# Kernel tuning notes

Measured on AMD Instinct MI355X. Metric: run time of the kernel, lower is better.

## Reference

```python
import jax, jax.numpy as jnp
import numpy as np

ORDER = 2
HIDDEN = 64
INPUT_SIZE = 2
N_NODES = 1024
BATCH = 8
STEPS = 32
GN_EPS = 1e-5


def setup_inputs() -> dict:
    key = jax.random.key(0)
    ks = jax.random.split(key, 8)
    c_gate_in = INPUT_SIZE + HIDDEN            # channels of concat([x, h]) fed to gate convs
    n_supp = 2 * ORDER                          # fwd/bwd row-normalized adj + (order-1) powers each
    c_conv = (n_supp + 1) * c_gate_in           # include_self=True adds the identity (self) block

    def w(k, shape, fan_in):
        s = 1.0 / np.sqrt(fan_in)
        return jax.random.uniform(k, shape, jnp.float32, -s, s)

    return {
        "x":   jax.random.normal(ks[0], (BATCH, INPUT_SIZE, N_NODES, STEPS), jnp.float32),
        "adj": jax.random.uniform(ks[1], (N_NODES, N_NODES), jnp.float32),
        "h0":  jax.random.normal(ks[2], (HIDDEN, N_NODES), jnp.float32) / np.sqrt(HIDDEN),
        "Wr": w(ks[3], (HIDDEN, c_conv), c_conv), "br": jnp.zeros((HIDDEN,), jnp.float32),
        "Wu": w(ks[4], (HIDDEN, c_conv), c_conv), "bu": jnp.zeros((HIDDEN,), jnp.float32),
        "Wc": w(ks[5], (HIDDEN, c_conv), c_conv), "bc": jnp.zeros((HIDDEN,), jnp.float32),
        "gamma": jnp.ones((HIDDEN,), jnp.float32), "beta": jnp.zeros((HIDDEN,), jnp.float32),
        "Wo": w(ks[6], (INPUT_SIZE, HIDDEN), HIDDEN), "bo": jnp.zeros((INPUT_SIZE,), jnp.float32),
    }


def _supports(adj, order):
    # SpatialConvOrderK.compute_support_orderK(adj, K, include_self=True)
    fwd = adj / (adj.sum(1, keepdims=True) + 1e-8)
    bwd = adj.T / (adj.T.sum(1, keepdims=True) + 1e-8)
    supp = [fwd, bwd]
    for a in (fwd, bwd):
        ak = a
        for _ in range(order - 1):
            ak = ak @ a.T               # higher-order diffusion; include_self -> keep diagonal
            supp.append(ak)
    return jnp.stack(supp)              # [S, n, n], S = 2*order


def _gconv(z, supp, W, b):
    # order-1 graph conv over precomputed order-K supports, include_self=True
    # z: [b, c, n]; supp: [S, n, n]; torch: einsum('ncvl,wv->ncwl')
    agg = jnp.einsum('bcv,swv->bscw', z, supp)            # [b, S, c, n]
    zc = jnp.concatenate([z[:, None], agg], axis=1)       # [b, S+1, c, n] (self first)
    zc = zc.reshape(z.shape[0], -1, z.shape[2])           # [b, (S+1)*c, n]
    return jnp.einsum('oc,bcn->bon', W, zc) + b[None, :, None]


def _gnorm(h, gamma, beta):
    # GroupNorm(num_groups=1): normalize each sample over (channels, nodes)
    m = h.mean(axis=(1, 2), keepdims=True)
    v = ((h - m) ** 2).mean(axis=(1, 2), keepdims=True)
    return (h - m) * jax.lax.rsqrt(v + GN_EPS) * gamma[None, :, None] + beta[None, :, None]


def reference(x, adj, h0, Wr, br, Wu, bu, Wc, bc, gamma, beta, Wo, bo):
    supp = _supports(adj, ORDER)
    b, _, n, _ = x.shape
    h = jnp.broadcast_to(h0[None], (b, HIDDEN, n))
    xs = jnp.moveaxis(x, -1, 0)                           # [steps, b, c_in, n]

    def step(h, xt):
        zg = jnp.concatenate([xt, h], axis=1)             # [b, c_in+hidden, n]
        r = jax.nn.sigmoid(_gconv(zg, supp, Wr, br))      # reset gate
        u = jax.nn.sigmoid(_gconv(zg, supp, Wu, bu))      # update gate
        zc = jnp.concatenate([xt, r * h], axis=1)
        c = jnp.tanh(_gconv(zc, supp, Wc, bc))            # candidate
        hn = _gnorm(u * h + (1.0 - u) * c, gamma, beta)   # norm applied post-cell (h[layer] = norm(...))
        x_hat = jnp.einsum('oc,bcn->bon', Wo, hn) + bo[None, :, None]  # first_stage 1x1 conv
        return hn, (x_hat, hn)

    _, (imps, hs) = jax.lax.scan(step, h, xs)
    imputations = jnp.moveaxis(imps, 0, -1)               # [b, input_size, n, steps]
    states = jnp.moveaxis(hs, 0, -1)[None]                # [n_layers=1, b, hidden, n, steps]
    return imputations, states
```

## Files before the change

kernel.cpp:

```cpp
#include <hip/hip_runtime.h>
#include <math.h>

#define NN 1024
#define HID 64
#define CIN 2
#define BB 8
#define TT 32
#define CG 66
#define NBC 528
#define K2 384
#define GN_EPS 1e-5f
#define LDAP 72

typedef __attribute__((ext_vector_type(8))) short short8v;
typedef __attribute__((ext_vector_type(4))) float float4v;

#define GLD16(gp, lp) __builtin_amdgcn_global_load_lds( \
    (const __attribute__((address_space(1))) void*)(gp), \
    (__attribute__((address_space(3))) void*)(lp), 16, 0, 0)

__device__ __forceinline__ unsigned short f2b(float v) {
    union { float f; unsigned int u; } a; a.f = v;
    unsigned int r = a.u + 0x7FFFu + ((a.u >> 16) & 1u);
    return (unsigned short)(r >> 16);
}
__device__ __forceinline__ float b2f(unsigned short b) {
    union { unsigned int u; float f; } a; a.u = ((unsigned int)b) << 16;
    return a.f;
}
__device__ __forceinline__ float sigmoidf_(float v) { return 1.f / (1.f + __expf(-v)); }

__device__ __forceinline__ float wave_reduce_sum(float v) {
    #pragma unroll
    for (int o = 32; o > 0; o >>= 1) v += __shfl_down(v, o, 64);
    return v;
}


__global__ void rowsum_k(const float* __restrict__ adj, float* __restrict__ rs) {
    int i = blockIdx.x;
    float s = 0.f;
    for (int j = threadIdx.x; j < NN; j += 256) s += adj[(size_t)i * NN + j];
    s = wave_reduce_sum(s);
    __shared__ float sh[4];
    int wid = threadIdx.x >> 6, lid = threadIdx.x & 63;
    if (lid == 0) sh[wid] = s;
    __syncthreads();
    if (threadIdx.x == 0) rs[i] = sh[0] + sh[1] + sh[2] + sh[3];
}

__global__ void colsum_k(const float* __restrict__ adj, float* __restrict__ cpart) {
    int j = (blockIdx.x & 3) * 256 + threadIdx.x;
    int r0 = (blockIdx.x >> 2) * 128;
    float s = 0.f;
    for (int i = 0; i < 128; i++) s += adj[(size_t)(r0 + i) * NN + j];
    cpart[(size_t)(blockIdx.x >> 2) * NN + j] = s;
}

__global__ void fwdb_k(const float* __restrict__ adj, const float* __restrict__ rs,
                       unsigned short* __restrict__ sb) {
    int idx = blockIdx.x * 256 + threadIdx.x;
    int i = idx >> 10;
    sb[idx] = f2b(adj[idx] / (rs[i] + 1e-8f));
}

__global__ void bwdb_k(const float* __restrict__ adj, const float* __restrict__ cpart,
                       unsigned short* __restrict__ sb) {
    __shared__ float tile[32][33];
    int i0 = blockIdx.y * 32, j0 = blockIdx.x * 32;
    int tx = threadIdx.x, ty = threadIdx.y;
    #pragma unroll
    for (int r = ty; r < 32; r += 8)
        tile[r][tx] = adj[(size_t)(j0 + r) * NN + i0 + tx];
    __syncthreads();
    #pragma unroll
    for (int r = ty; r < 32; r += 8) {
        int i = i0 + r;
        float cs = 0.f;
        #pragma unroll
        for (int c = 0; c < 8; c++) cs += cpart[(size_t)c * NN + i];
        sb[(size_t)i * NN + j0 + tx] = f2b(tile[tx][r] / (cs + 1e-8f));
    }
}

__global__ __launch_bounds__(256) void suppk_mfma(const unsigned short* __restrict__ sb,
                                                  unsigned short* __restrict__ outb) {
    int z = blockIdx.z;
    const unsigned short* A = sb + (size_t)z * NN * NN;
    unsigned short* D = outb + (size_t)z * NN * NN;
    __shared__ unsigned short lA[128 * LDAP];
    __shared__ unsigned short lB[64 * LDAP];
    int tid = threadIdx.x;
    int m0 = blockIdx.x * 128, n0 = blockIdx.y * 64;
    int lane = tid & 63, wave = tid >> 6;
    int wm = wave >> 1, wn = wave & 1;
    float4v acc[4][2];
    #pragma unroll
    for (int i = 0; i < 4; i++)
        #pragma unroll
        for (int j = 0; j < 2; j++) acc[i][j] = (float4v){0.f, 0.f, 0.f, 0.f};
    int lrow = lane & 15, lk8 = (lane >> 4) * 8;
    for (int k0 = 0; k0 < NN; k0 += 64) {
        #pragma unroll
        for (int s = 0; s < 4; s++) {
            int slot = tid + s * 256;
            int r = slot >> 3, kg = slot & 7;
            *(short8v*)(lA + r * LDAP + kg * 8) =
                *(const short8v*)(A + (size_t)(m0 + r) * NN + k0 + kg * 8);
        }
        #pragma unroll
        for (int s = 0; s < 2; s++) {
            int slot = tid + s * 256;
            int r = slot >> 3, kg = slot & 7;
            *(short8v*)(lB + r * LDAP + kg * 8) =
                *(const short8v*)(A + (size_t)(n0 + r) * NN + k0 + kg * 8);
        }
        __syncthreads();
        #pragma unroll
        for (int kk = 0; kk < 2; kk++) {
            short8v af[4], bf[2];
            #pragma unroll
            for (int i = 0; i < 4; i++)
                af[i] = *(const short8v*)(lA + (wm * 64 + i * 16 + lrow) * LDAP + kk * 32 + lk8);
            #pragma unroll
            for (int j = 0; j < 2; j++)
                bf[j] = *(const short8v*)(lB + (wn * 32 + j * 16 + lrow) * LDAP + kk * 32 + lk8);
            #pragma unroll
            for (int i = 0; i < 4; i++)
                #pragma unroll
                for (int j = 0; j < 2; j++)
                    acc[i][j] = __builtin_amdgcn_mfma_f32_16x16x32_bf16(af[i], bf[j], acc[i][j], 0, 0, 0);
        }
        __syncthreads();
    }
    int col = lane & 15, q4 = (lane >> 4) * 4;
    #pragma unroll
    for (int i = 0; i < 4; i++)
        #pragma unroll
        for (int j = 0; j < 2; j++) {
            int n = n0 + wn * 32 + j * 16 + col;
            #pragma unroll
            for (int r = 0; r < 4; r++) {
                int mm = m0 + wm * 64 + i * 16 + q4 + r;
                D[(size_t)mm * NN + n] = f2b(acc[i][j][r]);
            }
        }
}

__global__ void wconv_k(const float* __restrict__ Wr, const float* __restrict__ Wu,
                        const float* __restrict__ Wc, unsigned short* __restrict__ Wb,
                        unsigned short* __restrict__ Wcb) {
    int idx = blockIdx.x * 256 + threadIdx.x;
    int row = idx / K2, j = idx - row * K2;
    float v = 0.f;
    if (j < 330) {
        int q = j / CG, rr = j - q * CG;
        int chan = q * CG + (rr < HID ? rr + CIN : rr - HID);
        if (row < 64) v = Wr[row * 330 + chan];
        else if (row < 128) v = Wu[(row - 64) * 330 + chan];
        else v = Wc[(row - 128) * 330 + chan];
    }
    if (row < 128) Wb[row * K2 + j] = f2b(v);
    else Wcb[(row - 128) * K2 + j] = f2b(v);
}

__global__ void zeroz_k(unsigned short* __restrict__ z) {
    size_t i = ((size_t)blockIdx.x * 256 + threadIdx.x) * 8;
    *(short8v*)(z + i) = (short8v){0, 0, 0, 0, 0, 0, 0, 0};
}

__global__ void init_k(const float* __restrict__ x, const float* __restrict__ h0,
                       float* __restrict__ h, unsigned short* __restrict__ Z2g,
                       unsigned short* __restrict__ Z2c, unsigned short* __restrict__ Abfg,
                       unsigned short* __restrict__ Abfc) {
    int m = blockIdx.x * 256 + threadIdx.x;
    int b = m >> 10, n = m & 1023;
    for (int c = 0; c < HID; c++) {
        float v = h0[(c << 10) + n];
        h[(size_t)m * HID + c] = v;
        unsigned short hv = f2b(v);
        Z2g[(size_t)m * K2 + c] = hv;
        Abfg[(((size_t)(b * CG + c)) << 10) | n] = hv;
    }
    for (int o = 0; o < CIN; o++) {
        float xv = x[((((size_t)(b * CIN + o)) << 10) + n) * TT];
        unsigned short xb = f2b(xv);
        Z2g[(size_t)m * K2 + HID + o] = xb;
        Z2c[(size_t)m * K2 + HID + o] = xb;
        Abfg[(((size_t)(b * CG + HID + o)) << 10) | n] = xb;
        Abfc[(((size_t)(b * CG + HID + o)) << 10) | n] = xb;
    }
}


__global__ __launch_bounds__(256) void agg2_k(const unsigned short* __restrict__ S,
                                              const unsigned short* __restrict__ Abf,
                                              unsigned short* __restrict__ Z2) {
    __shared__ __align__(16) unsigned short lA[3][64 * 64];
    __shared__ __align__(16) unsigned short lB[3][64 * 64];
    int tid = threadIdx.x;
    int lin = blockIdx.y * 9 + blockIdx.x;
    int swz = (lin & 7) * 72 + (lin >> 3);
    int c0 = (swz % 9) * 64;
    int m0 = (swz / 9) * 64;
    int lane = tid & 63, wave = tid >> 6;
    int wm = wave >> 1, wn = wave & 1;
    float4v acc[2][2];
    #pragma unroll
    for (int i = 0; i < 2; i++)
        #pragma unroll
        for (int j = 0; j < 2; j++) acc[i][j] = (float4v){0.f, 0.f, 0.f, 0.f};
    int lrow = lane & 15, hi = lane >> 4;

    auto stage = [&](unsigned short* bufA, unsigned short* bufB, int k0) {
        #pragma unroll
        for (int i = 0; i < 2; i++) {
            int cid = (i * 4 + wave) * 64 + lane;
            int r = cid >> 3, sz = cid & 7;
            GLD16(S + (size_t)(m0 + r) * NN + k0 + ((sz ^ (r & 7)) << 3),
                  bufA + (i * 4 + wave) * 512);
        }
        #pragma unroll
        for (int i = 0; i < 2; i++) {
            int cid = (i * 4 + wave) * 64 + lane;
            int r = cid >> 3, sz = cid & 7;
            GLD16(Abf + (((size_t)(c0 + r)) << 10) + k0 + ((sz ^ (r & 7)) << 3),
                  bufB + (i * 4 + wave) * 512);
        }
    };

    unsigned short *a0 = lA[0], *a1 = lA[1], *a2 = lA[2];
    unsigned short *b0 = lB[0], *b1 = lB[1], *b2 = lB[2];
    stage(a0, b0, 0);
    stage(a1, b1, 64);
    for (int kt = 0; kt < 16; kt++) {
        if (kt < 15) asm volatile("s_waitcnt vmcnt(4)" ::: "memory");
        else         asm volatile("s_waitcnt vmcnt(0)" ::: "memory");
        __builtin_amdgcn_s_barrier();
        asm volatile("" ::: "memory");
        if (kt < 14) stage(a2, b2, (kt + 2) * 64);
        #pragma unroll
        for (int kk = 0; kk < 2; kk++) {
            int cb = kk * 4 + hi;
            short8v af[2], bf[2];
            #pragma unroll
            for (int i = 0; i < 2; i++) {
                int lr = wm * 32 + i * 16 + lrow;
                af[i] = *(const short8v*)(a0 + lr * 64 + ((cb ^ (lr & 7)) << 3));
            }
            #pragma unroll
            for (int j = 0; j < 2; j++) {
                int lr = wn * 32 + j * 16 + lrow;
                bf[j] = *(const short8v*)(b0 + lr * 64 + ((cb ^ (lr & 7)) << 3));
            }
            #pragma unroll
            for (int i = 0; i < 2; i++)
                #pragma unroll
                for (int j = 0; j < 2; j++)
                    acc[i][j] = __builtin_amdgcn_mfma_f32_16x16x32_bf16(af[i], bf[j], acc[i][j], 0, 0, 0);
        }
        { unsigned short* t = a0; a0 = a1; a1 = a2; a2 = t; }
        { unsigned short* t = b0; b0 = b1; b1 = b2; b2 = t; }
    }
    int col = lane & 15, q4 = (lane >> 4) * 4;
    int s_idx = m0 >> 10;
    int nb0 = (m0 & 1023) + wm * 32;
    #pragma unroll
    for (int j = 0; j < 2; j++) {
        int bc = c0 + wn * 32 + j * 16 + col;
        if (bc < NBC) {
            int b = bc / CG;
            int rr = bc - b * CG;
            size_t zcol = (size_t)CG + s_idx * CG + rr;
            #pragma unroll
            for (int i = 0; i < 2; i++) {
                int nb = nb0 + i * 16 + q4;
                #pragma unroll
                for (int r = 0; r < 4; r++)
                    Z2[((size_t)((b << 10) | (nb + r))) * K2 + zcol] = f2b(acc[i][j][r]);
            }
        }
    }
}

__global__ __launch_bounds__(256) void gates_k2(const unsigned short* __restrict__ Z2g,
                                                const unsigned short* __restrict__ Wb,
                                                const float* __restrict__ br,
                                                const float* __restrict__ bu,
                                                const float* __restrict__ h,
                                                float* __restrict__ u,
                                                unsigned short* __restrict__ Z2c,
                                                unsigned short* __restrict__ Abfc) {
    __shared__ __align__(16) unsigned short lA[3][32 * 64];
    __shared__ __align__(16) unsigned short lB[3][64 * 64];
    int tid = threadIdx.x;
    int m0 = blockIdx.x * 32;
    int isU = blockIdx.y;
    const unsigned short* W = Wb + (size_t)isU * 64 * K2;
    int lane = tid & 63, wave = tid >> 6;
    int wm = wave >> 1, wn = wave & 1;
    float4v acc[2];
    acc[0] = (float4v){0.f, 0.f, 0.f, 0.f};
    acc[1] = (float4v){0.f, 0.f, 0.f, 0.f};
    int lrow = lane & 15, hi = lane >> 4;

    auto stage = [&](unsigned short* bufA, unsigned short* bufB, int k0) {
        {
            int cid = wave * 64 + lane;
            int r = cid >> 3, sz = cid & 7;
            GLD16(Z2g + (size_t)(m0 + r) * K2 + k0 + ((sz ^ (r & 7)) << 3),
                  bufA + wave * 512);
        }
        #pragma unroll
        for (int i = 0; i < 2; i++) {
            int cid = (i * 4 + wave) * 64 + lane;
            int r = cid >> 3, sz = cid & 7;
            GLD16(W + (size_t)r * K2 + k0 + ((sz ^ (r & 7)) << 3),
                  bufB + (i * 4 + wave) * 512);
        }
    };

    unsigned short *a0 = lA[0], *a1 = lA[1], *a2 = lA[2];
    unsigned short *b0 = lB[0], *b1 = lB[1], *b2 = lB[2];
    stage(a0, b0, 0);
    stage(a1, b1, 64);
    for (int kt = 0; kt < 6; kt++) {
        if (kt < 5) asm volatile("s_waitcnt vmcnt(3)" ::: "memory");
        else        asm volatile("s_waitcnt vmcnt(0)" ::: "memory");
        __builtin_amdgcn_s_barrier();
        asm volatile("" ::: "memory");
        if (kt < 4) stage(a2, b2, (kt + 2) * 64);
        #pragma unroll
        for (int kk = 0; kk < 2; kk++) {
            int cb = kk * 4 + hi;
            short8v af, bf[2];
            {
                int lr = wm * 16 + lrow;
                af = *(const short8v*)(a0 + lr * 64 + ((cb ^ (lr & 7)) << 3));
            }
            #pragma unroll
            for (int j = 0; j < 2; j++) {
                int lr = wn * 32 + j * 16 + lrow;
                bf[j] = *(const short8v*)(b0 + lr * 64 + ((cb ^ (lr & 7)) << 3));
            }
            #pragma unroll
            for (int j = 0; j < 2; j++)
                acc[j] = __builtin_amdgcn_mfma_f32_16x16x32_bf16(af, bf[j], acc[j], 0, 0, 0);
        }
        { unsigned short* t = a0; a0 = a1; a1 = a2; a2 = t; }
        { unsigned short* t = b0; b0 = b1; b1 = b2; b2 = t; }
    }
    int col = lane & 15, q4 = (lane >> 4) * 4;
    #pragma unroll
    for (int j = 0; j < 2; j++) {
        int oo = wn * 32 + j * 16 + col;
        float bias = isU ? bu[oo] : br[oo];
        #pragma unroll
        for (int r = 0; r < 4; r++) {
            int m = m0 + wm * 16 + q4 + r;
            float g = sigmoidf_(acc[j][r] + bias);
            if (isU) {
                u[(size_t)m * HID + oo] = g;
            } else {
                float rh = g * h[(size_t)m * HID + oo];
                unsigned short hv = f2b(rh);
                Z2c[(size_t)m * K2 + oo] = hv;
                int b = m >> 10, n = m & 1023;
                Abfc[(((size_t)(b * CG + oo)) << 10) | n] = hv;
            }
        }
    }
}

__global__ __launch_bounds__(256) void cand_k2(const unsigned short* __restrict__ Z2c,
                                               const unsigned short* __restrict__ Wcb,
                                               const float* __restrict__ bcv,
                                               const float* __restrict__ u,
                                               const float* __restrict__ h,
                                               float* __restrict__ hraw,
                                               float* __restrict__ stats2, int t) {
    __shared__ __align__(16) unsigned short lA[3][32 * 64];
    __shared__ __align__(16) unsigned short lB[3][64 * 64];
    int tid = threadIdx.x;
    int m0 = blockIdx.x * 32;
    int lane = tid & 63, wave = tid >> 6;
    int wm = wave >> 1, wn = wave & 1;
    float4v acc[2];
    acc[0] = (float4v){0.f, 0.f, 0.f, 0.f};
    acc[1] = (float4v){0.f, 0.f, 0.f, 0.f};
    int lrow = lane & 15, hi = lane >> 4;

    auto stage = [&](unsigned short* bufA, unsigned short* bufB, int k0) {
        {
            int cid = wave * 64 + lane;
            int r = cid >> 3, sz = cid & 7;
            GLD16(Z2c + (size_t)(m0 + r) * K2 + k0 + ((sz ^ (r & 7)) << 3),
                  bufA + wave * 512);
        }
        #pragma unroll
        for (int i = 0; i < 2; i++) {
            int cid = (i * 4 + wave) * 64 + lane;
            int r = cid >> 3, sz = cid & 7;
            GLD16(Wcb + (size_t)r * K2 + k0 + ((sz ^ (r & 7)) << 3),
                  bufB + (i * 4 + wave) * 512);
        }
    };

    unsigned short *a0 = lA[0], *a1 = lA[1], *a2 = lA[2];
    unsigned short *b0 = lB[0], *b1 = lB[1], *b2 = lB[2];
    stage(a0, b0, 0);
    stage(a1, b1, 64);
    for (int kt = 0; kt < 6; kt++) {
        if (kt < 5) asm volatile("s_waitcnt vmcnt(3)" ::: "memory");
        else        asm volatile("s_waitcnt vmcnt(0)" ::: "memory");
        __builtin_amdgcn_s_barrier();
        asm volatile("" ::: "memory");
        if (kt < 4) stage(a2, b2, (kt + 2) * 64);
        #pragma unroll
        for (int kk = 0; kk < 2; kk++) {
            int cb = kk * 4 + hi;
            short8v af, bf[2];
            {
                int lr = wm * 16 + lrow;
                af = *(const short8v*)(a0 + lr * 64 + ((cb ^ (lr & 7)) << 3));
            }
            #pragma unroll
            for (int j = 0; j < 2; j++) {
                int lr = wn * 32 + j * 16 + lrow;
                bf[j] = *(const short8v*)(b0 + lr * 64 + ((cb ^ (lr & 7)) << 3));
            }
            #pragma unroll
            for (int j = 0; j < 2; j++)
                acc[j] = __builtin_amdgcn_mfma_f32_16x16x32_bf16(af, bf[j], acc[j], 0, 0, 0);
        }
        { unsigned short* t_ = a0; a0 = a1; a1 = a2; a2 = t_; }
        { unsigned short* t_ = b0; b0 = b1; b1 = b2; b2 = t_; }
    }
    int col = lane & 15, q4 = (lane >> 4) * 4;
    float ls = 0.f, ls2 = 0.f;
    #pragma unroll
    for (int j = 0; j < 2; j++) {
        int oo = wn * 32 + j * 16 + col;
        float bias = bcv[oo];
        #pragma unroll
        for (int r = 0; r < 4; r++) {
            int m = m0 + wm * 16 + q4 + r;
            float cv = tanhf(acc[j][r] + bias);
            float uv = u[(size_t)m * HID + oo];
            float hv = h[(size_t)m * HID + oo];
            float hr = uv * hv + (1.f - uv) * cv;
            hraw[(size_t)m * HID + oo] = hr;
            ls += hr;
            ls2 = fmaf(hr, hr, ls2);
        }
    }
    ls = wave_reduce_sum(ls);
    ls2 = wave_reduce_sum(ls2);
    __shared__ float sred[8];
    if (lane == 0) { sred[wave] = ls; sred[4 + wave] = ls2; }
    __syncthreads();
    if (tid == 0) {
        float S = sred[0] + sred[1] + sred[2] + sred[3];
        float S2 = sred[4] + sred[5] + sred[6] + sred[7];
        int b = blockIdx.x >> 5, slot = blockIdx.x & 31;
        float* dst = stats2 + (((size_t)t * BB + b) * 32 + slot) * 2;
        dst[0] = S;
        dst[1] = S2;
    }
}

__global__ __launch_bounds__(256) void apply_k2(const float* __restrict__ hraw,
                                                const float* __restrict__ stats2,
                                                const float* __restrict__ gamma,
                                                const float* __restrict__ beta,
                                                const float* __restrict__ Wo,
                                                const float* __restrict__ bo,
                                                const float* __restrict__ x,
                                                float* __restrict__ h,
                                                unsigned short* __restrict__ Z2g,
                                                unsigned short* __restrict__ Z2c,
                                                unsigned short* __restrict__ Abfg,
                                                unsigned short* __restrict__ Abfc,
                                                unsigned short* __restrict__ hseq8,
                                                float* __restrict__ iseq, int t) {
    int gid = blockIdx.x * 256 + threadIdx.x;
    int m = gid >> 3, q = gid & 7;
    int b = m >> 10, n = m & 1023;
    const float* st = stats2 + ((size_t)t * BB + b) * 64;
    float S = 0.f, S2 = 0.f;
    #pragma unroll
    for (int i = 0; i < 16; i++) {
        float4 p4 = *(const float4*)&st[i * 4];
        S += p4.x + p4.z;
        S2 += p4.y + p4.w;
    }
    float mean = S * (1.f / 65536.f);
    float rstd = rsqrtf(S2 * (1.f / 65536.f) - mean * mean + GN_EPS);
    bool more = (t < TT - 1);
    int c0 = q * 8;
    float v[8];
    unsigned short hb[8];
    #pragma unroll
    for (int k = 0; k < 8; k += 4) {
        float4 r4 = *(const float4*)&hraw[(size_t)m * HID + c0 + k];
        v[k + 0] = (r4.x - mean) * rstd * gamma[c0 + k + 0] + beta[c0 + k + 0];
        v[k + 1] = (r4.y - mean) * rstd * gamma[c0 + k + 1] + beta[c0 + k + 1];
        v[k + 2] = (r4.z - mean) * rstd * gamma[c0 + k + 2] + beta[c0 + k + 2];
        v[k + 3] = (r4.w - mean) * rstd * gamma[c0 + k + 3] + beta[c0 + k + 3];
    }
    float acc0 = 0.f, acc1 = 0.f;
    #pragma unroll
    for (int k = 0; k < 8; k++) {
        acc0 = fmaf(Wo[c0 + k], v[k], acc0);
        acc1 = fmaf(Wo[HID + c0 + k], v[k], acc1);
        hb[k] = f2b(v[k]);
    }
    short8v h8;
    #pragma unroll
    for (int k = 0; k < 8; k++) h8[k] = (short)hb[k];
    size_t hsbase = ((size_t)(t & 7) * 8192 + m) * HID + c0;
    *(short8v*)&hseq8[hsbase] = h8;
    if (more) {
        #pragma unroll
        for (int k = 0; k < 8; k += 4)
            *(float4*)&h[(size_t)m * HID + c0 + k] = make_float4(v[k], v[k + 1], v[k + 2], v[k + 3]);
        *(short8v*)&Z2g[(size_t)m * K2 + c0] = h8;
        #pragma unroll
        for (int k = 0; k < 8; k++)
            Abfg[(((size_t)(b * CG + c0 + k)) << 10) | n] = hb[k];
    }
    acc0 += __shfl_xor(acc0, 1, 64); acc0 += __shfl_xor(acc0, 2, 64); acc0 += __shfl_xor(acc0, 4, 64);
    acc1 += __shfl_xor(acc1, 1, 64); acc1 += __shfl_xor(acc1, 2, 64); acc1 += __shfl_xor(acc1, 4, 64);
    if (q == 0) {
        iseq[((size_t)t * 8192 + m) * 2 + 0] = acc0 + bo[0];
        iseq[((size_t)t * 8192 + m) * 2 + 1] = acc1 + bo[1];
        if (more) {
            #pragma unroll
            for (int o = 0; o < CIN; o++) {
                float xv = x[((((size_t)(b * CIN + o)) << 10) + n) * TT + t + 1];
                unsigned short xb = f2b(xv);
                Z2g[(size_t)m * K2 + HID + o] = xb;
                Z2c[(size_t)m * K2 + HID + o] = xb;
                Abfg[(((size_t)(b * CG + HID + o)) << 10) | n] = xb;
                Abfc[(((size_t)(b * CG + HID + o)) << 10) | n] = xb;
            }
        }
    }
}

__global__ __launch_bounds__(256) void strans_k(const unsigned short* __restrict__ hseq8,
                                                float* __restrict__ outS, int t0) {
    __shared__ unsigned short lt[8 * 576];
    int tid = threadIdx.x;
    int b = blockIdx.x >> 7;
    int n0 = (blockIdx.x & 127) * 8;
    #pragma unroll
    for (int s = 0; s < 2; s++) {
        int slot = tid + s * 256;
        int tt = slot >> 6, dn = (slot >> 3) & 7, kc = slot & 7;
        short8v vv = *(const short8v*)(hseq8 + ((size_t)tt * 8192 + ((b << 10) | (n0 + dn))) * HID + kc * 8);
        *(short8v*)(lt + tt * 576 + dn * 72 + kc * 8) = vv;
    }
    __syncthreads();
    #pragma unroll
    for (int s = 0; s < 2; s++) {
        int rid = tid + s * 256;
        int c = rid >> 3, dn = rid & 7;
        float f[8];
        #pragma unroll
        for (int tt = 0; tt < 8; tt++) f[tt] = b2f(lt[tt * 576 + dn * 72 + c]);
        float* dst = outS + ((((size_t)(b * HID + c)) << 10) + n0 + dn) * TT + t0;
        *(float4*)&dst[0] = make_float4(f[0], f[1], f[2], f[3]);
        *(float4*)&dst[4] = make_float4(f[4], f[5], f[6], f[7]);
    }
}

__global__ void itrans_k(const float* __restrict__ iseq, float* __restrict__ out) {
    int gid = blockIdx.x * 256 + threadIdx.x;
    int b = gid >> 11, o = (gid >> 10) & 1, n = gid & 1023;
    float f[TT];
    #pragma unroll
    for (int t = 0; t < TT; t++)
        f[t] = iseq[((size_t)t * 8192 + ((b << 10) | n)) * 2 + o];
    float* dst = out + ((((size_t)(b * CIN + o)) << 10) + n) * TT;
    #pragma unroll
    for (int k = 0; k < TT; k += 4)
        *(float4*)&dst[k] = make_float4(f[k], f[k + 1], f[k + 2], f[k + 3]);
}


extern "C" void kernel_launch(void* const* d_in, const int* in_sizes, int n_in,
                              void* d_out, int out_size, void* d_ws, size_t ws_size,
                              hipStream_t stream) {
    const float* x     = (const float*)d_in[0];
    const float* adj   = (const float*)d_in[1];
    const float* h0    = (const float*)d_in[2];
    const float* Wr    = (const float*)d_in[3];
    const float* br    = (const float*)d_in[4];
    const float* Wu    = (const float*)d_in[5];
    const float* bu    = (const float*)d_in[6];
    const float* Wc    = (const float*)d_in[7];
    const float* bcv   = (const float*)d_in[8];
    const float* gamma = (const float*)d_in[9];
    const float* beta  = (const float*)d_in[10];
    const float* Wo    = (const float*)d_in[11];
    const float* bo    = (const float*)d_in[12];
    float* out = (float*)d_out;

    char* p = (char*)d_ws;
    unsigned short* suppb = (unsigned short*)p;  p += (size_t)4 * NN * NN * 2;
    unsigned short* Abfg  = (unsigned short*)p;  p += (size_t)576 * NN * 2;
    unsigned short* Abfc  = (unsigned short*)p;  p += (size_t)576 * NN * 2;
    unsigned short* Z2g   = (unsigned short*)p;  p += (size_t)8192 * K2 * 2;
    unsigned short* Z2c   = (unsigned short*)p;  p += (size_t)8192 * K2 * 2;
    unsigned short* Wb    = (unsigned short*)p;  p += (size_t)128 * K2 * 2;
    unsigned short* Wcb   = (unsigned short*)p;  p += (size_t)64 * K2 * 2;
    float* u     = (float*)p;  p += (size_t)8192 * HID * 4;
    float* h     = (float*)p;  p += (size_t)8192 * HID * 4;
    float* hraw  = (float*)p;  p += (size_t)8192 * HID * 4;
    unsigned short* hseq8 = (unsigned short*)p;  p += (size_t)8 * 8192 * HID * 2;
    float* iseq  = (float*)p;  p += (size_t)TT * 8192 * 2 * 4;
    float* rowsum = (float*)p; p += NN * 4;
    float* cpart  = (float*)p; p += (size_t)8 * NN * 4;
    float* stats2 = (float*)p; p += (size_t)TT * BB * 32 * 2 * 4;

    float* outS = out + (size_t)BB * CIN * NN * TT;

    rowsum_k<<<NN, 256, 0, stream>>>(adj, rowsum);
    colsum_k<<<32, 256, 0, stream>>>(adj, cpart);
    fwdb_k<<<(NN * NN) / 256, 256, 0, stream>>>(adj, rowsum, suppb);
    bwdb_k<<<dim3(32, 32), dim3(32, 8), 0, stream>>>(adj, cpart, suppb + (size_t)NN * NN);
    suppk_mfma<<<dim3(8, 16, 2), 256, 0, stream>>>(suppb, suppb + (size_t)2 * NN * NN);
    wconv_k<<<(192 * K2) / 256, 256, 0, stream>>>(Wr, Wu, Wc, Wb, Wcb);
    zeroz_k<<<(2 * 8192 * K2) / (8 * 256), 256, 0, stream>>>(Z2g);
    init_k<<<8192 / 256, 256, 0, stream>>>(x, h0, h, Z2g, Z2c, Abfg, Abfc);

    for (int t = 0; t < TT; t++) {
        agg2_k<<<dim3(9, 64), 256, 0, stream>>>(suppb, Abfg, Z2g);
        gates_k2<<<dim3(256, 2), 256, 0, stream>>>(Z2g, Wb, br, bu, h, u, Z2c, Abfc);
        agg2_k<<<dim3(9, 64), 256, 0, stream>>>(suppb, Abfc, Z2c);
        cand_k2<<<256, 256, 0, stream>>>(Z2c, Wcb, bcv, u, h, hraw, stats2, t);
        apply_k2<<<256, 256, 0, stream>>>(hraw, stats2, gamma, beta, Wo, bo, x, h,
                                          Z2g, Z2c, Abfg, Abfc, hseq8, iseq, t);
        if ((t & 7) == 7)
            strans_k<<<1024, 256, 0, stream>>>(hseq8, outS, t - 7);
    }
    itrans_k<<<64, 256, 0, stream>>>(iseq, out);
}
```

Measured before the change: 1.544 ms.

## Fuse candidate GEMM and group-norm apply via per-batch atomic barrier

Merges the candidate-gate kernel and the norm/apply kernel into one launch. The pre-norm hidden tile is kept in LDS instead of going through global memory. Group-norm statistics are exchanged through a per-batch atomic counter that each block spins on until all 32 blocks of that batch have arrived. This removes one launch per step and the global round trip of hraw, but it relies on all 256 blocks being co-resident, since a missing block would deadlock the spin-wait.

```diff
diff --git a/kernel.cpp b/kernel.cpp
--- a/kernel.cpp
+++ b/kernel.cpp
@@ -372,15 +372,26 @@
     }
 }
 
-__global__ __launch_bounds__(256) void cand_k2(const unsigned short* __restrict__ Z2c,
-                                               const unsigned short* __restrict__ Wcb,
-                                               const float* __restrict__ bcv,
-                                               const float* __restrict__ u,
-                                               const float* __restrict__ h,
-                                               float* __restrict__ hraw,
-                                               float* __restrict__ stats2, int t) {
+__global__ __launch_bounds__(256) void candapply_k(unsigned short* Z2c,
+                                                   const unsigned short* __restrict__ Wcb,
+                                                   const float* __restrict__ bcv,
+                                                   const float* __restrict__ u,
+                                                   float* h,
+                                                   const float* __restrict__ gamma,
+                                                   const float* __restrict__ beta,
+                                                   const float* __restrict__ Wo,
+                                                   const float* __restrict__ bo,
+                                                   const float* __restrict__ x,
+                                                   unsigned short* __restrict__ Z2g,
+                                                   unsigned short* __restrict__ Abfg,
+                                                   unsigned short* __restrict__ Abfc,
+                                                   unsigned short* __restrict__ hseq8,
+                                                   float* __restrict__ iseq,
+                                                   float* __restrict__ stats2,
+                                                   unsigned* __restrict__ cnt, int t) {
     __shared__ __align__(16) unsigned short lA[3][32 * 64];
     __shared__ __align__(16) unsigned short lB[3][64 * 64];
+    __shared__ float sred[8];
     int tid = threadIdx.x;
     int m0 = blockIdx.x * 32;
     int lane = tid & 63, wave = tid >> 6;
@@ -436,6 +447,8 @@
         { unsigned short* t_ = a0; a0 = a1; a1 = a2; a2 = t_; }
         { unsigned short* t_ = b0; b0 = b1; b1 = b2; b2 = t_; }
     }
+    __syncthreads();
+    float* lds_h = (float*)lA;
     int col = lane & 15, q4 = (lane >> 4) * 4;
     float ls = 0.f, ls2 = 0.f;
     #pragma unroll
@@ -444,48 +457,35 @@
         float bias = bcv[oo];
         #pragma unroll
         for (int r = 0; r < 4; r++) {
-            int m = m0 + wm * 16 + q4 + r;
+            int mrel = wm * 16 + q4 + r;
+            int m = m0 + mrel;
             float cv = tanhf(acc[j][r] + bias);
             float uv = u[(size_t)m * HID + oo];
             float hv = h[(size_t)m * HID + oo];
             float hr = uv * hv + (1.f - uv) * cv;
-            hraw[(size_t)m * HID + oo] = hr;
+            lds_h[mrel * 65 + oo] = hr;
             ls += hr;
             ls2 = fmaf(hr, hr, ls2);
         }
     }
     ls = wave_reduce_sum(ls);
     ls2 = wave_reduce_sum(ls2);
-    __shared__ float sred[8];
     if (lane == 0) { sred[wave] = ls; sred[4 + wave] = ls2; }
     __syncthreads();
+    int b = blockIdx.x >> 5, slot = blockIdx.x & 31;
     if (tid == 0) {
         float S = sred[0] + sred[1] + sred[2] + sred[3];
         float S2 = sred[4] + sred[5] + sred[6] + sred[7];
-        int b = blockIdx.x >> 5, slot = blockIdx.x & 31;
         float* dst = stats2 + (((size_t)t * BB + b) * 32 + slot) * 2;
-        dst[0] = S;
-        dst[1] = S2;
-    }
-}
-
-__global__ __launch_bounds__(256) void apply_k2(const float* __restrict__ hraw,
-                                                const float* __restrict__ stats2,
-                                                const float* __restrict__ gamma,
-                                                const float* __restrict__ beta,
-                                                const float* __restrict__ Wo,
-                                                const float* __restrict__ bo,
-                                                const float* __restrict__ x,
-                                                float* __restrict__ h,
-                                                unsigned short* __restrict__ Z2g,
-                                                unsigned short* __restrict__ Z2c,
-                                                unsigned short* __restrict__ Abfg,
-                                                unsigned short* __restrict__ Abfc,
-                                                unsigned short* __restrict__ hseq8,
-                                                float* __restrict__ iseq, int t) {
-    int gid = blockIdx.x * 256 + threadIdx.x;
-    int m = gid >> 3, q = gid & 7;
-    int b = m >> 10, n = m & 1023;
+        __hip_atomic_store(dst + 0, S, __ATOMIC_RELAXED, __HIP_MEMORY_SCOPE_AGENT);
+        __hip_atomic_store(dst + 1, S2, __ATOMIC_RELAXED, __HIP_MEMORY_SCOPE_AGENT);
+        __hip_atomic_fetch_add(&cnt[t * 8 + b], 1u, __ATOMIC_RELEASE, __HIP_MEMORY_SCOPE_AGENT);
+        while (__hip_atomic_load(&cnt[t * 8 + b], __ATOMIC_RELAXED, __HIP_MEMORY_SCOPE_AGENT) < 32u)
+            __builtin_amdgcn_s_sleep(8);
+    }
+    __syncthreads();
+    asm volatile("" ::: "memory");
+
     const float* st = stats2 + ((size_t)t * BB + b) * 64;
     float S = 0.f, S2 = 0.f;
     #pragma unroll
@@ -497,16 +497,16 @@
     float mean = S * (1.f / 65536.f);
     float rstd = rsqrtf(S2 * (1.f / 65536.f) - mean * mean + GN_EPS);
     bool more = (t < TT - 1);
+    int mrel2 = tid >> 3, q = tid & 7;
+    int m = m0 + mrel2;
+    int n = m & 1023;
     int c0 = q * 8;
     float v[8];
     unsigned short hb[8];
     #pragma unroll
-    for (int k = 0; k < 8; k += 4) {
-        float4 r4 = *(const float4*)&hraw[(size_t)m * HID + c0 + k];
-        v[k + 0] = (r4.x - mean) * rstd * gamma[c0 + k + 0] + beta[c0 + k + 0];
-        v[k + 1] = (r4.y - mean) * rstd * gamma[c0 + k + 1] + beta[c0 + k + 1];
-        v[k + 2] = (r4.z - mean) * rstd * gamma[c0 + k + 2] + beta[c0 + k + 2];
-        v[k + 3] = (r4.w - mean) * rstd * gamma[c0 + k + 3] + beta[c0 + k + 3];
+    for (int k = 0; k < 8; k++) {
+        float raw = lds_h[mrel2 * 65 + c0 + k];
+        v[k] = (raw - mean) * rstd * gamma[c0 + k] + beta[c0 + k];
     }
     float acc0 = 0.f, acc1 = 0.f;
     #pragma unroll
@@ -617,14 +617,16 @@
     unsigned short* Wcb   = (unsigned short*)p;  p += (size_t)64 * K2 * 2;
     float* u     = (float*)p;  p += (size_t)8192 * HID * 4;
     float* h     = (float*)p;  p += (size_t)8192 * HID * 4;
-    float* hraw  = (float*)p;  p += (size_t)8192 * HID * 4;
     unsigned short* hseq8 = (unsigned short*)p;  p += (size_t)8 * 8192 * HID * 2;
     float* iseq  = (float*)p;  p += (size_t)TT * 8192 * 2 * 4;
     float* rowsum = (float*)p; p += NN * 4;
     float* cpart  = (float*)p; p += (size_t)8 * NN * 4;
     float* stats2 = (float*)p; p += (size_t)TT * BB * 32 * 2 * 4;
+    unsigned* cnt = (unsigned*)p; p += 1024;
 
     float* outS = out + (size_t)BB * CIN * NN * TT;
+
+    hipMemsetAsync(cnt, 0, 1024, stream);
 
     rowsum_k<<<NN, 256, 0, stream>>>(adj, rowsum);
     colsum_k<<<32, 256, 0, stream>>>(adj, cpart);
@@ -639,9 +641,9 @@
         agg2_k<<<dim3(9, 64), 256, 0, stream>>>(suppb, Abfg, Z2g);
         gates_k2<<<dim3(256, 2), 256, 0, stream>>>(Z2g, Wb, br, bu, h, u, Z2c, Abfc);
         agg2_k<<<dim3(9, 64), 256, 0, stream>>>(suppb, Abfc, Z2c);
-        cand_k2<<<256, 256, 0, stream>>>(Z2c, Wcb, bcv, u, h, hraw, stats2, t);
-        apply_k2<<<256, 256, 0, stream>>>(hraw, stats2, gamma, beta, Wo, bo, x, h,
-                                          Z2g, Z2c, Abfg, Abfc, hseq8, iseq, t);
+        candapply_k<<<256, 256, 0, stream>>>(Z2c, Wcb, bcv, u, h, gamma, beta, Wo, bo,
+                                             x, Z2g, Abfg, Abfc, hseq8, iseq,
+                                             stats2, cnt, t);
         if ((t & 7) == 7)
             strans_k<<<1024, 256, 0, stream>>>(hseq8, outS, t - 7);
     }
```

Measured after the change: 1.760 ms. 14.0% more time.

## Split gate kernel and co-schedule update-gate GEMM with candidate aggregation

Applied to the files above, without the earlier changes.

The combined reset/update gate kernel is split. The reset gate runs alone because the candidate aggregation needs r*h. The update-gate GEMM is merged into the same launch as the second aggregation, dispatched by block index, so the two independent pieces of work share the GPU and fill idle CUs. The cost is one extra kernel body with larger shared-memory allocation for the gate blocks, and a heterogeneous grid that may cause tail imbalance.

```diff
diff --git a/kernel.cpp b/kernel.cpp
--- a/kernel.cpp
+++ b/kernel.cpp
@@ -193,13 +193,11 @@
 }
 
 
-__global__ __launch_bounds__(256) void agg2_k(const unsigned short* __restrict__ S,
-                                              const unsigned short* __restrict__ Abf,
-                                              unsigned short* __restrict__ Z2) {
-    __shared__ __align__(16) unsigned short lA[3][64 * 64];
-    __shared__ __align__(16) unsigned short lB[3][64 * 64];
+__device__ __forceinline__ void agg_body(int lin, const unsigned short* __restrict__ S,
+                                         const unsigned short* __restrict__ Abf,
+                                         unsigned short* __restrict__ Z2,
+                                         unsigned short (*lA)[4096], unsigned short (*lB)[4096]) {
     int tid = threadIdx.x;
-    int lin = blockIdx.y * 9 + blockIdx.x;
     int swz = (lin & 7) * 72 + (lin >> 3);
     int c0 = (swz % 9) * 64;
     int m0 = (swz / 9) * 64;
@@ -283,19 +281,17 @@
     }
 }
 
-__global__ __launch_bounds__(256) void gates_k2(const unsigned short* __restrict__ Z2g,
-                                                const unsigned short* __restrict__ Wb,
-                                                const float* __restrict__ br,
-                                                const float* __restrict__ bu,
-                                                const float* __restrict__ h,
-                                                float* __restrict__ u,
-                                                unsigned short* __restrict__ Z2c,
-                                                unsigned short* __restrict__ Abfc) {
-    __shared__ __align__(16) unsigned short lA[3][32 * 64];
-    __shared__ __align__(16) unsigned short lB[3][64 * 64];
+__device__ __forceinline__ void gate_body(int m0, int isU,
+                                          const unsigned short* __restrict__ Z2g,
+                                          const unsigned short* __restrict__ Wb,
+                                          const float* __restrict__ br,
+                                          const float* __restrict__ bu,
+                                          const float* __restrict__ h,
+                                          float* __restrict__ u,
+                                          unsigned short* __restrict__ Z2c,
+                                          unsigned short* __restrict__ Abfc,
+                                          unsigned short (*lA)[4096], unsigned short (*lB)[4096]) {
     int tid = threadIdx.x;
-    int m0 = blockIdx.x * 32;
-    int isU = blockIdx.y;
     const unsigned short* W = Wb + (size_t)isU * 64 * K2;
     int lane = tid & 63, wave = tid >> 6;
     int wm = wave >> 1, wn = wave & 1;
@@ -370,6 +366,42 @@
             }
         }
     }
+}
+
+__global__ __launch_bounds__(256) void agg2_k(const unsigned short* __restrict__ S,
+                                              const unsigned short* __restrict__ Abf,
+                                              unsigned short* __restrict__ Z2) {
+    __shared__ __align__(16) unsigned short lA[3][4096];
+    __shared__ __align__(16) unsigned short lB[3][4096];
+    agg_body(blockIdx.y * 9 + blockIdx.x, S, Abf, Z2, lA, lB);
+}
+
+__global__ __launch_bounds__(256) void gates_r_k(const unsigned short* __restrict__ Z2g,
+                                                 const unsigned short* __restrict__ Wb,
+                                                 const float* __restrict__ br,
+                                                 const float* __restrict__ h,
+                                                 unsigned short* __restrict__ Z2c,
+                                                 unsigned short* __restrict__ Abfc) {
+    __shared__ __align__(16) unsigned short lA[3][4096];
+    __shared__ __align__(16) unsigned short lB[3][4096];
+    gate_body(blockIdx.x * 32, 0, Z2g, Wb, br, (const float*)0, h, (float*)0,
+              Z2c, Abfc, lA, lB);
+}
+
+__global__ __launch_bounds__(256) void aggu_k(const unsigned short* __restrict__ S,
+                                              const unsigned short* __restrict__ Abfc,
+                                              unsigned short* __restrict__ Z2c,
+                                              const unsigned short* __restrict__ Z2g,
+                                              const unsigned short* __restrict__ Wb,
+                                              const float* __restrict__ bu,
+                                              float* __restrict__ u) {
+    __shared__ __align__(16) unsigned short lA[3][4096];
+    __shared__ __align__(16) unsigned short lB[3][4096];
+    if (blockIdx.x < 576)
+        agg_body(blockIdx.x, S, Abfc, Z2c, lA, lB);
+    else
+        gate_body((blockIdx.x - 576) * 32, 1, Z2g, Wb, (const float*)0, bu,
+                  (const float*)0, u, (unsigned short*)0, (unsigned short*)0, lA, lB);
 }
 
 __global__ __launch_bounds__(256) void cand_k2(const unsigned short* __restrict__ Z2c,
@@ -637,8 +669,8 @@
 
     for (int t = 0; t < TT; t++) {
         agg2_k<<<dim3(9, 64), 256, 0, stream>>>(suppb, Abfg, Z2g);
-        gates_k2<<<dim3(256, 2), 256, 0, stream>>>(Z2g, Wb, br, bu, h, u, Z2c, Abfc);
-        agg2_k<<<dim3(9, 64), 256, 0, stream>>>(suppb, Abfc, Z2c);
+        gates_r_k<<<256, 256, 0, stream>>>(Z2g, Wb, br, h, Z2c, Abfc);
+        aggu_k<<<832, 256, 0, stream>>>(suppb, Abfc, Z2c, Z2g, Wb, bu, u);
         cand_k2<<<256, 256, 0, stream>>>(Z2c, Wcb, bcv, u, h, hraw, stats2, t);
         apply_k2<<<256, 256, 0, stream>>>(hraw, stats2, gamma, beta, Wo, bo, x, h,
                                           Z2g, Z2c, Abfg, Abfc, hseq8, iseq, t);
```

Result: faster. 1.380 ms (-10.6%).
